# Kernel tuning notes

Hardware: AMD Instinct MI355X
Metric: run time of the kernel (lower is better)

## Reference

```python
import jax, jax.numpy as jnp
import numpy as np
from jax import lax

B, H, W = 2, 960, 1280
K = 1024            # max_keypoints
P = 256             # num_pairs (BAD descriptor dim)
NUM_SCALES = 3
DIFF_ITERS = 3
KAPPA = 0.05
TAU = 0.2           # explicit FED step size (stable < 0.25)
DET_THRESHOLD = 0.001
AKAZE_NMS = 5       # detector-internal NMS window
NMS_WIN = 2 * 3 + 1 # pipeline NMS window (nms_radius=3)
ORI_PATCH = 15
ORI_SIGMA = 2.5
SINK_ITERS = 20
EPSILON = 1.0
UNUSED_SCORE = 1.0
MAX_RADIUS = 5

def _conv(x, k):
    return lax.conv_general_dilated(x, k, (1, 1), 'SAME', dimension_numbers=('NCHW', 'OIHW', 'NCHW'))

_sob = np.array([[-1., 0., 1.], [-2., 0., 2.], [-1., 0., 1.]], np.float32) / 8.0
KX = jnp.asarray(_sob)[None, None]
KY = jnp.asarray(_sob.T)[None, None]
_d2 = np.array([[0., 0., 0.], [1., -2., 1.], [0., 0., 0.]], np.float32)
KXX = jnp.asarray(_d2)[None, None]
KYY = jnp.asarray(_d2.T)[None, None]

# Gaussian weighting kernel for orientation estimation
_c = np.arange(ORI_PATCH, dtype=np.float32) - (ORI_PATCH - 1) / 2.0
_gy, _gx = np.meshgrid(_c, _c, indexing='ij')
_g = np.exp(-(_gx ** 2 + _gy ** 2) / (2.0 * ORI_SIGMA ** 2))
GK = jnp.asarray((_g / _g.sum()).astype(np.float32))[None, None]

# Box-average kernel bank: one normalized box filter per radius 0..MAX_RADIUS
_bc = np.arange(-MAX_RADIUS, MAX_RADIUS + 1, dtype=np.float32)
_by, _bx = np.meshgrid(_bc, _bc, indexing='ij')
_rv = np.arange(MAX_RADIUS + 1, dtype=np.float32)[:, None, None]
_bm = ((np.abs(_by) <= _rv) & (np.abs(_bx) <= _rv)).astype(np.float32)
BOX_BANK = jnp.asarray((_bm / (2.0 * _rv + 1.0) ** 2)[:, None])  # [R+1,1,11,11]

def _shifts(a):
    p = jnp.pad(a, ((0, 0), (0, 0), (1, 1), (1, 1)), mode='edge')
    return p[:, :, :-2, 1:-1], p[:, :, 2:, 1:-1], p[:, :, 1:-1, :-2], p[:, :, 1:-1, 2:]

def _fed_step(L):
    # One explicit Perona-Malik (FED) nonlinear diffusion step
    Lx = _conv(L, KX); Ly = _conv(L, KY)
    g = 1.0 / (1.0 + (Lx * Lx + Ly * Ly) / (KAPPA * KAPPA))
    Ln, Ls, Lw, Le = _shifts(L)
    gn, gs, gw, ge = _shifts(g)
    flux = 0.5 * ((g + gn) * (Ln - L) + (g + gs) * (Ls - L) + (g + gw) * (Lw - L) + (g + ge) * (Le - L))
    return L + TAU * flux

def _maxpool(s, win):
    return lax.reduce_window(s, -jnp.inf, lax.max, (1, win, win), (1, 1, 1), 'SAME')

def _akaze(img):
    # Multi-scale FED diffusion -> Hessian determinant response + orientation map
    L = img
    resp = jnp.zeros((B, H, W), img.dtype)
    for _s in range(NUM_SCALES):
        for _i in range(DIFF_ITERS):
            L = _fed_step(L)
        Lxx = _conv(L, KXX); Lyy = _conv(L, KYY); Lxy = _conv(_conv(L, KX), KY)
        resp = jnp.maximum(resp, (Lxx * Lyy - Lxy * Lxy)[:, 0])
    resp = jnp.where(resp > DET_THRESHOLD, resp, 0.0)
    resp = resp * (resp >= _maxpool(resp, AKAZE_NMS) - 1e-7).astype(resp.dtype)
    gxs = _conv(_conv(img, KX), GK)[:, 0]
    gys = _conv(_conv(img, KY), GK)[:, 0]
    theta = jnp.arctan2(gys, gxs)  # [B,H,W]
    return resp, theta

def _select(resp):
    # Pipeline-level maxpool NMS + top-K selection, pad invalid with (-1,-1)
    mask = (resp >= _maxpool(resp, NMS_WIN) - 1e-7).astype(resp.dtype)
    s = resp * mask
    s = jnp.where(s > 0.0, s, 0.0)
    tk, idx = lax.top_k(s.reshape(B, -1), K)
    y = (idx // W).astype(jnp.float32)
    x = (idx % W).astype(jnp.float32)
    valid = (tk > 0.0).astype(jnp.float32)
    kpts = jnp.where(valid[..., None] > 0.5, jnp.stack([y, x], -1), -1.0)
    return kpts, tk * valid, valid

def _bad(img, kpts, theta, valid, offsets, radii, thresholds):
    # Orientation-aware BAD: box-averaged intensity differences at rotated pair offsets
    bank = _conv(img, BOX_BANK)  # [B,R+1,H,W]
    yc = jnp.clip(kpts[..., 0], 0.0, H - 1.0)
    xc = jnp.clip(kpts[..., 1], 0.0, W - 1.0)
    yi = jnp.round(yc).astype(jnp.int32); xi = jnp.round(xc).astype(jnp.int32)
    th = jax.vmap(lambda m, a, b: m[a, b])(theta, yi, xi)  # [B,K] nearest-sampled orientation
    c = jnp.cos(th)[..., None]; s = jnp.sin(th)[..., None]
    ox1, oy1, ox2, oy2 = offsets[:, 0], offsets[:, 1], offsets[:, 2], offsets[:, 3]
    px1 = xc[..., None] + c * ox1 - s * oy1
    py1 = yc[..., None] + s * ox1 + c * oy1
    px2 = xc[..., None] + c * ox2 - s * oy2
    py2 = yc[..., None] + s * ox2 + c * oy2
    rb = jnp.broadcast_to(radii[None, :], (K, P))
    def samp(px, py):
        xi_ = jnp.clip(jnp.round(px), 0, W - 1).astype(jnp.int32)
        yi_ = jnp.clip(jnp.round(py), 0, H - 1).astype(jnp.int32)
        return jax.vmap(lambda bk, a, b: bk[rb, a, b])(bank, yi_, xi_)  # [B,K,P]
    v = (samp(px1, py1) - samp(px2, py2)) - thresholds[None, None, :]
    v = v * valid[..., None]
    n = jnp.linalg.norm(v, axis=-1, keepdims=True)
    return v / (n + 1e-8)

def _sinkhorn(d1, d2):
    sq1 = jnp.sum(d1 * d1, -1); sq2 = jnp.sum(d2 * d2, -1)
    dist2 = sq1[:, :, None] + sq2[:, None, :] - 2.0 * jnp.einsum('bip,bjp->bij', d1, d2)
    dist = jnp.sqrt(jnp.maximum(dist2, 0.0) + 1e-12)
    Z = jnp.full((B, K + 1, K + 1), UNUSED_SCORE, d1.dtype)
    Z = Z.at[:, :K, :K].set(-dist) / EPSILON
    norm = -jnp.log(2.0 * K)
    log_mu = jnp.concatenate([jnp.zeros(K, Z.dtype), jnp.log(float(K)) * jnp.ones(1, Z.dtype)]) + norm
    log_nu = log_mu
    def body(carry, _):
        u, v = carry
        u = log_mu[None] - jax.nn.logsumexp(Z + v[:, None, :], axis=2)
        v = log_nu[None] - jax.nn.logsumexp(Z + u[:, :, None], axis=1)
        return (u, v), None
    (u, v), _ = lax.scan(body, (jnp.zeros((B, K + 1), Z.dtype), jnp.zeros((B, K + 1), Z.dtype)), None, length=SINK_ITERS)
    return jnp.exp(Z + u[:, :, None] + v[:, None, :] - norm)  # [B,K+1,K+1]

def _forward(img1, img2, offsets, thresholds, radii):
    r1, t1 = _akaze(img1)
    r2, t2 = _akaze(img2)
    k1, s1, v1 = _select(r1)
    k2, s2, v2 = _select(r2)
    d1 = _bad(img1, k1, t1, v1, offsets, radii, thresholds)
    d2 = _bad(img2, k2, t2, v2, offsets, radii, thresholds)
    probs = _sinkhorn(d1, d2)
    return k1, k2, probs

def setup_inputs():
    key = jax.random.key(0)
    k1, k2, k3, k4, k5 = jax.random.split(key, 5)
    img1 = jax.random.uniform(k1, (B, 1, H, W), jnp.float32)
    img2 = jax.random.uniform(k2, (B, 1, H, W), jnp.float32)
    offsets = jax.random.uniform(k3, (P, 4), jnp.float32, -16.0, 16.0)  # box_params - 16
    thresholds = 0.05 * jax.random.normal(k5, (P,), jnp.float32)
    radii = jax.random.randint(k4, (P,), 0, MAX_RADIUS + 1, jnp.int32)
    return {'img1': img1, 'img2': img2, 'offsets': offsets, 'thresholds': thresholds, 'radii': radii}

def reference(img1, img2, offsets, thresholds, radii):
    return _forward(img1, img2, offsets, thresholds, radii)
```

## Files before the change

kernel.cpp:

```cpp
#include <hip/hip_runtime.h>
#include <hip/hip_fp16.h>
#include <math.h>

typedef unsigned long long u64;
typedef unsigned int u32;

#define Hh 960
#define Ww 1280
#define Bb 2
#define Kk 1024
#define Pp 256
#define KP1 1025
#define NSEG 4
#define LISTCAP 131072
#define PR 28
#define PS 57
#define ZLD 1040
#define CANDCAP 8192
static const size_t ZB = (size_t)KP1*ZLD;

static const size_t HWp = (size_t)Hh * Ww;
static const size_t PLn = HWp * Bb;

#define TAUf 0.2f
#define NMS_EPS 1e-7f
#define DET_T 0.001f
#define NORMV (-7.6246189861593985f)
#define LOGKV (6.9314718055994531f)

__constant__ float WR[6] = {1.0f, 1.0f/9.0f, 1.0f/25.0f, 1.0f/49.0f, 1.0f/81.0f, 1.0f/121.0f};

__device__ __forceinline__ int imin(int a,int b){return a<b?a:b;}
__device__ __forceinline__ int imax(int a,int b){return a>b?a:b;}

__global__ __launch_bounds__(256) void fed_step(const float* __restrict__ src, float* __restrict__ dst){
  __shared__ float Lt[36][37];
  __shared__ float Gt[34][35];
  const int bx = blockIdx.x*32, by = blockIdx.y*32, b = blockIdx.z;
  const float* S = src + (size_t)b*HWp;
  float* D = dst + (size_t)b*HWp;
  const int t = threadIdx.y*32 + threadIdx.x;
  for (int i=t;i<36*36;i+=256){
    int ly=i/36, lx=i-ly*36;
    int gy=by+ly-2, gx=bx+lx-2;
    Lt[ly][lx] = (gy>=0 && gy<Hh && gx>=0 && gx<Ww) ? S[(size_t)gy*Ww+gx] : 0.0f;
  }
  __syncthreads();
  const float k2 = (float)(0.05*0.05);
  for (int i=t;i<34*34;i+=256){
    int ly=i/34, lx=i-ly*34;
    int Ly=ly+1, Lx=lx+1;
    float sx = (-Lt[Ly-1][Lx-1]+Lt[Ly-1][Lx+1]
                -2.0f*Lt[Ly][Lx-1]+2.0f*Lt[Ly][Lx+1]
                -Lt[Ly+1][Lx-1]+Lt[Ly+1][Lx+1])*0.125f;
    float sy = (-Lt[Ly-1][Lx-1]-2.0f*Lt[Ly-1][Lx]-Lt[Ly-1][Lx+1]
                +Lt[Ly+1][Lx-1]+2.0f*Lt[Ly+1][Lx]+Lt[Ly+1][Lx+1])*0.125f;
    Gt[ly][lx] = 1.0f/(1.0f + (sx*sx+sy*sy)/k2);
  }
  __syncthreads();
  for (int r=0;r<4;++r){
    int oy=threadIdx.y + r*8, ox=threadIdx.x;
    int gy=by+oy, gx=bx+ox;
    if (gy>=Hh || gx>=Ww) continue;
    int gyn=imax(gy-1,0), gys=imin(gy+1,Hh-1), gxw=imax(gx-1,0), gxe=imin(gx+1,Ww-1);
    float Lc=Lt[oy+2][ox+2];
    float Ln=Lt[gyn-by+2][ox+2];
    float Ls=Lt[gys-by+2][ox+2];
    float Lw=Lt[oy+2][gxw-bx+2];
    float Le=Lt[oy+2][gxe-bx+2];
    float gc=Gt[oy+1][ox+1];
    float gn=Gt[gyn-by+1][ox+1];
    float gs=Gt[gys-by+1][ox+1];
    float gw=Gt[oy+1][gxw-bx+1];
    float ge=Gt[oy+1][gxe-bx+1];
    float flux = 0.5f*((gc+gn)*(Ln-Lc) + (gc+gs)*(Ls-Lc) + (gc+gw)*(Lw-Lc) + (gc+ge)*(Le-Lc));
    D[(size_t)gy*Ww+gx] = Lc + TAUf*flux;
  }
}

__global__ __launch_bounds__(256) void fed_step_resp(const float* __restrict__ src, float* __restrict__ dstL,
                                                     float* __restrict__ resp, int first){
  __shared__ float Lt[40][41];
  __shared__ float Gt[38][39];
  __shared__ float Lp[36][37];
  const int bx=blockIdx.x*32, by=blockIdx.y*32, b=blockIdx.z;
  const int gx0=bx-4, gy0=by-4;
  const float* S=src+(size_t)b*HWp;
  float* DL=dstL+(size_t)b*HWp;
  float* R=resp+(size_t)b*HWp;
  const int t=threadIdx.y*32+threadIdx.x;
  const float k2=(float)(0.05*0.05);
  for(int i=t;i<40*40;i+=256){
    int ly=i/40, lx=i-(i/40)*40;
    int gy=gy0+ly, gx=gx0+lx;
    Lt[ly][lx]=(gy>=0&&gy<Hh&&gx>=0&&gx<Ww)?S[(size_t)gy*Ww+gx]:0.0f;
  }
  __syncthreads();
  for(int i=t;i<38*38;i+=256){
    int y=i/38+1, x=i-(i/38)*38+1;
    float sx=(-Lt[y-1][x-1]+Lt[y-1][x+1]
              -2.0f*Lt[y][x-1]+2.0f*Lt[y][x+1]
              -Lt[y+1][x-1]+Lt[y+1][x+1])*0.125f;
    float sy=(-Lt[y-1][x-1]-2.0f*Lt[y-1][x]-Lt[y-1][x+1]
              +Lt[y+1][x-1]+2.0f*Lt[y+1][x]+Lt[y+1][x+1])*0.125f;
    Gt[y-1][x-1]=1.0f/(1.0f+(sx*sx+sy*sy)/k2);
  }
  __syncthreads();
  for(int i=t;i<36*36;i+=256){
    int y=i/36+2, x=i-(i/36)*36+2;
    int gy=gy0+y, gx=gx0+x;
    float v=0.0f;
    if(gy>=0&&gy<Hh&&gx>=0&&gx<Ww){
      int yn=imax(gy-1,0)-gy0, ys=imin(gy+1,Hh-1)-gy0;
      int xw=imax(gx-1,0)-gx0, xe=imin(gx+1,Ww-1)-gx0;
      float Lc=Lt[y][x];
      float Ln=Lt[yn][x], Ls=Lt[ys][x], Lw=Lt[y][xw], Le=Lt[y][xe];
      float gc=Gt[y-1][x-1], gn=Gt[yn-1][x-1], gs=Gt[ys-1][x-1], gw=Gt[y-1][xw-1], ge=Gt[y-1][xe-1];
      float flux=0.5f*((gc+gn)*(Ln-Lc)+(gc+gs)*(Ls-Lc)+(gc+gw)*(Lw-Lc)+(gc+ge)*(Le-Lc));
      v=Lc+TAUf*flux;
    }
    Lp[y-2][x-2]=v;
  }
  __syncthreads();
  for(int i=t;i<32*32;i+=256){
    int oy=i>>5, ox=i&31;
    DL[(size_t)(by+oy)*Ww+(bx+ox)]=Lp[oy+2][ox+2];
  }
  for(int i=t;i<34*34;i+=256){
    int y=i/34+1, x=i-(i/34)*34+1;
    int gy=gy0+2+y, gx=gx0+2+x;
    float v=0.0f;
    if(gy>=0&&gy<Hh&&gx>=0&&gx<Ww){
      v=(-Lp[y-1][x-1]+Lp[y-1][x+1]
         -2.0f*Lp[y][x-1]+2.0f*Lp[y][x+1]
         -Lp[y+1][x-1]+Lp[y+1][x+1])*0.125f;
    }
    Gt[y-1][x-1]=v;
  }
  __syncthreads();
  for(int i=t;i<32*32;i+=256){
    int oy=i>>5, ox=i&31;
    int y=oy+2, x=ox+2;
    float Lxx=Lp[y][x-1]-2.0f*Lp[y][x]+Lp[y][x+1];
    float Lyy=Lp[y-1][x]-2.0f*Lp[y][x]+Lp[y+1][x];
    float Lxy=(-Gt[y-2][x-2]-2.0f*Gt[y-2][x-1]-Gt[y-2][x]
               +Gt[y][x-2]+2.0f*Gt[y][x-1]+Gt[y][x])*0.125f;
    float det=Lxx*Lyy-Lxy*Lxy;
    size_t id=(size_t)(by+oy)*Ww+(bx+ox);
    R[id]=first?fmaxf(det,0.0f):fmaxf(R[id],det);
  }
}

__global__ __launch_bounds__(256) void detect_compact(const float* __restrict__ resp,
                                                      u64* __restrict__ lists,
                                                      int* __restrict__ cnt, int segbase){
  const int TS=42;
  __shared__ float Tt[TS][TS+1];
  __shared__ float Ss[38][39];
  __shared__ u64 keys[1024];
  __shared__ int lcnt, gbase;
  const int bx = blockIdx.x*32, by = blockIdx.y*32, b = blockIdx.z;
  const float* S = resp + (size_t)b*HWp;
  const int t = threadIdx.y*32 + threadIdx.x;
  if (t==0) lcnt=0;
  for (int i=t;i<TS*TS;i+=256){
    int ly=i/TS, lx=i-ly*TS;
    int gy=by+ly-5, gx=bx+lx-5;
    float v = (gy>=0 && gy<Hh && gx>=0 && gx<Ww) ? S[(size_t)gy*Ww+gx] : 0.0f;
    Tt[ly][lx] = (v>DET_T) ? v : 0.0f;
  }
  __syncthreads();
  for (int i=t;i<38*38;i+=256){
    int ly=i/38, lx=i-ly*38;
    int ty=ly+2, tx=lx+2;
    float m=0.0f;
    #pragma unroll
    for(int dy=-2;dy<=2;dy++)
      #pragma unroll
      for(int dx=-2;dx<=2;dx++)
        m=fmaxf(m,Tt[ty+dy][tx+dx]);
    float c=Tt[ty][tx];
    Ss[ly][lx]=(c>=m-NMS_EPS)?c:0.0f;
  }
  __syncthreads();
  const int seg=segbase+b;
  for (int r=0;r<4;++r){
    int oy=threadIdx.y + r*8, ox=threadIdx.x;
    int gy=by+oy, gx=bx+ox;
    bool pos=false; u64 key=0;
    if (gy<Hh && gx<Ww){
      float v=Ss[oy+3][ox+3];
      if (v>0.0f){
        float m=0.0f;
        #pragma unroll
        for(int dy=0;dy<7;dy++)
          #pragma unroll
          for(int dx=0;dx<7;dx++)
            m=fmaxf(m,Ss[oy+dy][ox+dx]);
        if (v>=m-NMS_EPS){
          u32 idx=(u32)(gy*Ww+gx);
          key=((u64)__float_as_uint(v)<<32)|(u64)(0xFFFFFFFFu-idx);
          pos=true;
        }
      }
    }
    u64 mask=__ballot(pos);
    if (mask){
      int lane=t&63;
      int leader=__ffsll((long long)mask)-1;
      int base=0;
      if (lane==leader) base=atomicAdd(&lcnt,__popcll(mask));
      base=__shfl(base,leader);
      if (pos){
        int rk=__popcll(mask & ((1ULL<<lane)-1ULL));
        keys[base+rk]=key;
      }
    }
  }
  __syncthreads();
  if (t==0 && lcnt>0) gbase=atomicAdd(&cnt[seg*64], lcnt);
  __syncthreads();
  int n=lcnt;
  for (int i=t;i<n;i+=256){
    int p=gbase+i;
    if (p<LISTCAP) lists[(size_t)seg*LISTCAP+p]=keys[i];
  }
}

__global__ __launch_bounds__(256) void topk_hist16(const u64* __restrict__ lists, const int* __restrict__ cnt,
                                                   u32* __restrict__ h16){
  int seg=blockIdx.y;
  int n=imin(cnt[seg*64],LISTCAP);
  const u64* L=lists+(size_t)seg*LISTCAP;
  u32* H=h16+(size_t)seg*65536;
  for(int i=blockIdx.x*256+threadIdx.x;i<n;i+=gridDim.x*256){
    u32 b=(u32)(L[i]>>48);
    atomicAdd(&H[b],1u);
  }
}

__global__ __launch_bounds__(1024) void topk_decide16(const u32* __restrict__ h16, const int* __restrict__ cnt,
                                                      int* __restrict__ b16o, int* __restrict__ krem16,
                                                      int* __restrict__ takeAll, u64* __restrict__ Tf){
  int seg=blockIdx.x, tid=threadIdx.x;
  __shared__ u32 sc[1024];
  const u32* H=h16+(size_t)seg*65536;
  int n=imin(cnt[seg*64],LISTCAP);
  if(n<=Kk){
    if(tid==0){ takeAll[seg]=1; Tf[seg]=1ULL; b16o[seg]=-1; }
    return;
  }
  u32 csum=0;
  u32 hl[64];
  #pragma unroll 8
  for(int j=0;j<64;j++){ hl[j]=H[tid*64+j]; csum+=hl[j]; }
  sc[tid]=csum;
  __syncthreads();
  for(int off=1;off<1024;off<<=1){
    u32 v=(tid+off<1024)?sc[tid+off]:0u;
    __syncthreads();
    sc[tid]+=v;
    __syncthreads();
  }
  u32 nxt=(tid<1023)?sc[tid+1]:0u;
  if(sc[tid]>=(u32)Kk && nxt<(u32)Kk){
    u32 run=nxt;
    for(int j=63;j>=0;j--){
      u32 c=hl[j];
      run+=c;
      if(run>=(u32)Kk){
        b16o[seg]=tid*64+j;
        krem16[seg]=Kk-(int)(run-c);
        takeAll[seg]=0;
        break;
      }
    }
  }
}

__global__ __launch_bounds__(256) void topk_compact(const u64* __restrict__ lists, const int* __restrict__ cnt,
                                                    const int* __restrict__ b16o, const int* __restrict__ takeAll,
                                                    u64* __restrict__ candbuf, int* __restrict__ candcnt){
  int seg=blockIdx.y;
  if(takeAll[seg]) return;
  int n=imin(cnt[seg*64],LISTCAP);
  const u64* L=lists+(size_t)seg*LISTCAP;
  u32 b16=(u32)b16o[seg];
  for(int i0=blockIdx.x*256;i0<n;i0+=gridDim.x*256){
    int i=i0+threadIdx.x;
    bool sel=false; u64 k=0;
    if(i<n){ k=L[i]; sel=((u32)(k>>48)==b16); }
    u64 mask=__ballot(sel);
    if(mask){
      int lane=threadIdx.x&63;
      int leader=__ffsll((long long)mask)-1;
      int base=0;
      if(lane==leader) base=atomicAdd(&candcnt[seg*64],__popcll(mask));
      base=__shfl(base,leader);
      if(sel){
        int p=base+__popcll(mask & ((1ULL<<lane)-1ULL));
        if(p<CANDCAP) candbuf[(size_t)seg*CANDCAP+p]=k;
      }
    }
  }
}

__global__ __launch_bounds__(1024) void topk_finish(const u64* __restrict__ lists, const int* __restrict__ cnt,
                                                    const u64* __restrict__ candbuf, const int* __restrict__ candcnt,
                                                    const int* __restrict__ b16o, const int* __restrict__ krem16,
                                                    const int* __restrict__ takeAll, u64* __restrict__ Tf){
  int seg=blockIdx.x, tid=threadIdx.x;
  if(takeAll[seg]) return;
  __shared__ u64 cands[CANDCAP];
  __shared__ u32 h[256], scan[256];
  __shared__ int bsel;
  int cc=candcnt[seg*64];
  u64 pfx=((u64)(u32)b16o[seg])<<48;
  int kr=krem16[seg];
  if(cc<=CANDCAP){
    for(int i=tid;i<cc;i+=1024) cands[i]=candbuf[(size_t)seg*CANDCAP+i];
    __syncthreads();
    for(int rd=0;rd<6;rd++){
      int shift=40-8*rd;
      u64 maskHi=~0ULL<<(shift+8);
      if(tid<256) h[tid]=0;
      __syncthreads();
      for(int i=tid;i<cc;i+=1024){
        u64 k=cands[i];
        if((k&maskHi)==pfx) atomicAdd(&h[(int)((k>>shift)&255ULL)],1u);
      }
      __syncthreads();
      if(tid<256) scan[tid]=h[tid];
      __syncthreads();
      for(int off=1;off<256;off<<=1){
        u32 v=0;
        if(tid<256 && tid+off<256) v=scan[tid+off];
        __syncthreads();
        if(tid<256) scan[tid]+=v;
        __syncthreads();
      }
      if(tid<256){
        bool ge=(scan[tid]>=(u32)kr);
        bool geN=(tid<255)?(scan[tid+1]>=(u32)kr):false;
        if(ge && !geN) bsel=tid;
      }
      __syncthreads();
      int b=bsel;
      int acc=(b<255)?(int)scan[b+1]:0;
      pfx |= ((u64)(u32)b)<<shift;
      kr -= acc;
      __syncthreads();
    }
  } else {
    int n=imin(cnt[seg*64],LISTCAP);
    const u64* L=lists+(size_t)seg*LISTCAP;
    for(int rd=0;rd<6;rd++){
      int shift=40-8*rd;
      u64 maskHi=~0ULL<<(shift+8);
      if(tid<256) h[tid]=0;
      __syncthreads();
      for(int i=tid;i<n;i+=1024){
        u64 k=L[i];
        if((k&maskHi)==pfx) atomicAdd(&h[(int)((k>>shift)&255ULL)],1u);
      }
      __syncthreads();
      if(tid<256) scan[tid]=h[tid];
      __syncthreads();
      for(int off=1;off<256;off<<=1){
        u32 v=0;
        if(tid<256 && tid+off<256) v=scan[tid+off];
        __syncthreads();
        if(tid<256) scan[tid]+=v;
        __syncthreads();
      }
      if(tid<256){
        bool ge=(scan[tid]>=(u32)kr);
        bool geN=(tid<255)?(scan[tid+1]>=(u32)kr):false;
        if(ge && !geN) bsel=tid;
      }
      __syncthreads();
      int b=bsel;
      int acc=(b<255)?(int)scan[b+1]:0;
      pfx |= ((u64)(u32)b)<<shift;
      kr -= acc;
      __syncthreads();
    }
  }
  if(tid==0) Tf[seg]=pfx;
}

__global__ __launch_bounds__(256) void topk_gather(const u64* __restrict__ lists, const int* __restrict__ cnt,
                                                   const u64* __restrict__ Tf, u64* __restrict__ selbuf,
                                                   int* __restrict__ selcnt){
  int seg=blockIdx.y;
  int n=imin(cnt[seg*64],LISTCAP);
  u64 T=Tf[seg];
  const u64* L=lists+(size_t)seg*LISTCAP;
  for(int i0=blockIdx.x*256;i0<n;i0+=gridDim.x*256){
    int i=i0+threadIdx.x;
    bool sel=false; u64 k=0;
    if(i<n){ k=L[i]; sel=(k>=T); }
    u64 mask=__ballot(sel);
    if(mask){
      int lane=threadIdx.x&63;
      int leader=__ffsll((long long)mask)-1;
      int base=0;
      if(lane==leader) base=atomicAdd(&selcnt[seg*64],__popcll(mask));
      base=__shfl(base,leader);
      if(sel){
        int p=base+__popcll(mask & ((1ULL<<lane)-1ULL));
        if(p<Kk) selbuf[(size_t)seg*Kk+p]=k;
      }
    }
  }
}

__global__ __launch_bounds__(1024) void finalize_kernel(const u64* __restrict__ selbuf, const int* __restrict__ selcnt,
                                int* __restrict__ kyi, int* __restrict__ kxi, float* __restrict__ kval,
                                float* __restrict__ outp){
  int seg=blockIdx.x, tid=threadIdx.x;
  __shared__ u64 a[1024];
  int n=selcnt[seg*64]; if(n>Kk)n=Kk;
  a[tid]=(tid<n)?selbuf[(size_t)seg*Kk+tid]:0ULL;
  __syncthreads();
  for(int k=2;k<=1024;k<<=1){
    for(int j=k>>1;j>0;j>>=1){
      int ixj=tid^j;
      if(ixj>tid){
        u64 x=a[tid], y=a[ixj];
        bool desc=((tid&k)==0);
        if(desc ? (x<y) : (x>y)){ a[tid]=y; a[ixj]=x; }
      }
      __syncthreads();
    }
  }
  u64 key=a[tid];
  bool val=(key!=0ULL);
  u32 idx=0xFFFFFFFFu-(u32)(key&0xFFFFFFFFULL);
  int y= val ? (int)(idx/Ww) : 0;
  int x= val ? (int)(idx%Ww) : 0;
  int mi=seg*Kk+tid;
  kyi[mi]=y; kxi[mi]=x; kval[mi]= val?1.0f:0.0f;
  int imi=seg>>1, bb=seg&1;
  float* ko=outp + (size_t)imi*(Bb*Kk*2) + ((size_t)bb*Kk+tid)*2;
  ko[0]= val ? (float)y : -1.0f;
  ko[1]= val ? (float)x : -1.0f;
}

__global__ void init_weights(float* wn){
  if(threadIdx.x==0 && blockIdx.x==0){
    double w[15]; double S=0.0;
    for(int i=0;i<15;i++){ double c=(double)i-7.0; w[i]=exp(-(c*c)/(2.0*2.5*2.5)); S+=w[i]; }
    for(int i=0;i<15;i++) wn[i]=(float)(w[i]/S);
  }
}

__global__ __launch_bounds__(256) void bad_kernel(const float* __restrict__ img1, const float* __restrict__ img2,
                           const float* __restrict__ offs, const float* __restrict__ thrv,
                           const int* __restrict__ rad, const float* __restrict__ wn,
                           const int* __restrict__ kyi, const int* __restrict__ kxi,
                           const float* __restrict__ kval,
                           float* __restrict__ d1, float* __restrict__ d2,
                           float* __restrict__ sq1, float* __restrict__ sq2){
  __shared__ float sat[PS+1][PS+2];
  __shared__ float sm[4], smx[4], smy[4];
  __shared__ float w15s[15];
  __shared__ float nsh, thsh;
  int seg=blockIdx.y, ki=blockIdx.x, p=threadIdx.x;
  const float* img=(seg<2?img1:img2)+(size_t)(seg&1)*HWp;
  int mi=seg*Kk+ki;
  int yci=kyi[mi], xci=kxi[mi];
  if(p<15) w15s[p]=wn[p];
  for (int i=p;i<PS+1;i+=256){ sat[0][i]=0.0f; sat[i][0]=0.0f; }
  if (p==0) sat[0][PS]=0.0f;
  for (int i=p;i<PS*PS;i+=256){
    int ly=i/PS, lx=i-ly*PS;
    int gy=yci-PR+ly, gx=xci-PR+lx;
    sat[ly+1][lx+1]=(gy>=0&&gy<Hh&&gx>=0&&gx<Ww)?img[(size_t)gy*Ww+gx]:0.0f;
  }
  __syncthreads();
  {
    float ax=0.0f, ay=0.0f;
    if(p<225){
      int du=p/15-7, dv=p-(p/15)*15-7;
      int yy=yci+du, xx=xci+dv;
      if(yy>=0&&yy<Hh&&xx>=0&&xx<Ww){
        int ly=du+PR+1, lx=dv+PR+1;
        float p00=sat[ly-1][lx-1], p01=sat[ly-1][lx], p02=sat[ly-1][lx+1];
        float p10=sat[ly][lx-1],                       p12=sat[ly][lx+1];
        float p20=sat[ly+1][lx-1], p21=sat[ly+1][lx], p22=sat[ly+1][lx+1];
        float sx=(-p00+p02-2.0f*p10+2.0f*p12-p20+p22)*0.125f;
        float sy=(-p00-2.0f*p01-p02+p20+2.0f*p21+p22)*0.125f;
        float wgt=w15s[du+7]*w15s[dv+7];
        ax=wgt*sx; ay=wgt*sy;
      }
    }
    for(int o=32;o;o>>=1){ ax+=__shfl_down(ax,o); ay+=__shfl_down(ay,o); }
    if((p&63)==0){ smx[p>>6]=ax; smy[p>>6]=ay; }
    __syncthreads();
    if(p==0) thsh=atan2f(smy[0]+smy[1]+smy[2]+smy[3], smx[0]+smx[1]+smx[2]+smx[3]);
  }
  __syncthreads();
  if (p<PS){
    float run=0.0f;
    for(int x=1;x<=PS;x++){ run+=sat[p+1][x]; sat[p+1][x]=run; }
  }
  __syncthreads();
  if (p<PS){
    float run=0.0f;
    for(int y=1;y<=PS;y++){ run+=sat[y][p+1]; sat[y][p+1]=run; }
  }
  __syncthreads();
  float yc=(float)yci, xc=(float)xci;
  float th=thsh;
  float c=cosf(th), s=sinf(th);
  float ox1=offs[p*4+0], oy1=offs[p*4+1], ox2=offs[p*4+2], oy2=offs[p*4+3];
  int r=rad[p];
  float w=WR[r];
  float px1=xc+c*ox1-s*oy1, py1=yc+s*ox1+c*oy1;
  float px2=xc+c*ox2-s*oy2, py2=yc+s*ox2+c*oy2;
  auto boxl=[&](float px,float py,int r_)->float{
    float rx=rintf(px), ry=rintf(py);
    int xi=(int)fminf(fmaxf(rx,0.0f),(float)(Ww-1));
    int yi=(int)fminf(fmaxf(ry,0.0f),(float)(Hh-1));
    int lx=xi-(xci-PR), ly=yi-(yci-PR);
    int y2=ly+r_+1, y1=ly-r_, x2=lx+r_+1, x1=lx-r_;
    return sat[y2][x2]-sat[y1][x2]-sat[y2][x1]+sat[y1][x1];
  };
  float s1=boxl(px1,py1,r)*w;
  float s2=boxl(px2,py2,r)*w;
  float v=(s1-s2-thrv[p])*kval[mi];
  float t=v*v;
  for(int o=32;o;o>>=1) t+=__shfl_down(t,o);
  if((p&63)==0) sm[p>>6]=t;
  __syncthreads();
  if(p==0) nsh=sqrtf(sm[0]+sm[1]+sm[2]+sm[3]);
  __syncthreads();
  float dv=v/(nsh+1e-8f);
  float* dd=(seg<2?d1:d2);
  dd[((size_t)(seg&1)*Kk+ki)*Pp+p]=dv;
  float t2=dv*dv;
  for(int o=32;o;o>>=1) t2+=__shfl_down(t2,o);
  __syncthreads();
  if((p&63)==0) sm[p>>6]=t2;
  __syncthreads();
  if(p==0){ float* sq=(seg<2?sq1:sq2); sq[(size_t)(seg&1)*Kk+ki]=sm[0]+sm[1]+sm[2]+sm[3]; }
}

__global__ __launch_bounds__(256) void dist_kernel(const float* __restrict__ d1, const float* __restrict__ d2,
                            const float* __restrict__ sq1, const float* __restrict__ sq2,
                            float* __restrict__ Zm, float* __restrict__ Zt){
  int b=blockIdx.z;
  int i0=blockIdx.y*64, j0=blockIdx.x*64;
  int tid=threadIdx.x;
  int tx=tid&15, ty=tid>>4;
  __shared__ float Ast[64][68], Bst[64][68];
  const float* D1=d1+(size_t)b*Kk*Pp;
  const float* D2=d2+(size_t)b*Kk*Pp;
  float acc[4][4]={};
  for(int p0=0;p0<Pp;p0+=64){
    for(int i=tid;i<64*16;i+=256){
      int row=i>>4, c4=(i&15)<<2;
      float4 va=*reinterpret_cast<const float4*>(&D1[(size_t)(i0+row)*Pp+p0+c4]);
      float4 vb=*reinterpret_cast<const float4*>(&D2[(size_t)(j0+row)*Pp+p0+c4]);
      Ast[c4+0][row]=va.x; Ast[c4+1][row]=va.y; Ast[c4+2][row]=va.z; Ast[c4+3][row]=va.w;
      Bst[c4+0][row]=vb.x; Bst[c4+1][row]=vb.y; Bst[c4+2][row]=vb.z; Bst[c4+3][row]=vb.w;
    }
    __syncthreads();
    #pragma unroll 8
    for(int kk=0;kk<64;++kk){
      float4 av=*reinterpret_cast<const float4*>(&Ast[kk][ty*4]);
      float4 bv=*reinterpret_cast<const float4*>(&Bst[kk][tx*4]);
      acc[0][0]=fmaf(av.x,bv.x,acc[0][0]); acc[0][1]=fmaf(av.x,bv.y,acc[0][1]);
      acc[0][2]=fmaf(av.x,bv.z,acc[0][2]); acc[0][3]=fmaf(av.x,bv.w,acc[0][3]);
      acc[1][0]=fmaf(av.y,bv.x,acc[1][0]); acc[1][1]=fmaf(av.y,bv.y,acc[1][1]);
      acc[1][2]=fmaf(av.y,bv.z,acc[1][2]); acc[1][3]=fmaf(av.y,bv.w,acc[1][3]);
      acc[2][0]=fmaf(av.z,bv.x,acc[2][0]); acc[2][1]=fmaf(av.z,bv.y,acc[2][1]);
      acc[2][2]=fmaf(av.z,bv.z,acc[2][2]); acc[2][3]=fmaf(av.z,bv.w,acc[2][3]);
      acc[3][0]=fmaf(av.w,bv.x,acc[3][0]); acc[3][1]=fmaf(av.w,bv.y,acc[3][1]);
      acc[3][2]=fmaf(av.w,bv.z,acc[3][2]); acc[3][3]=fmaf(av.w,bv.w,acc[3][3]);
    }
    __syncthreads();
  }
  int gi=i0+ty*4, gj=j0+tx*4;
  float si[4], sj[4];
  #pragma unroll
  for(int i=0;i<4;i++){ si[i]=sq1[b*Kk+gi+i]; sj[i]=sq2[b*Kk+gj+i]; }
  #pragma unroll
  for(int i=0;i<4;i++){
    #pragma unroll
    for(int j=0;j<4;j++){
      float dd=si[i]+sj[j]-2.0f*acc[i][j];
      float dist=sqrtf(fmaxf(dd,0.0f)+1e-12f);
      Zm[(size_t)b*ZB+(size_t)(gi+i)*ZLD+(gj+j)]=-dist;
      Zt[(size_t)b*ZB+(size_t)(gj+j)*ZLD+(gi+i)]=-dist;
    }
  }
}

__global__ void zborder_kernel(float* __restrict__ Zm, float* __restrict__ Zt){
  int i=blockIdx.x*256+threadIdx.x;
  if(i>=Bb*KP1) return;
  int b=i/KP1, j=i-(i/KP1)*KP1;
  size_t base=(size_t)b*ZB;
  Zm[base+(size_t)j*ZLD+Kk]=1.0f;
  Zm[base+(size_t)Kk*ZLD+j]=1.0f;
  Zt[base+(size_t)j*ZLD+Kk]=1.0f;
  Zt[base+(size_t)Kk*ZLD+j]=1.0f;
  for(int c=KP1;c<ZLD;c++){
    Zm[base+(size_t)j*ZLD+c]=-1.0e30f;
    Zt[base+(size_t)j*ZLD+c]=-1.0e30f;
  }
}

__global__ void expz_kernel(const float* __restrict__ Zm, const float* __restrict__ Zt,
                            __half* __restrict__ Em, __half* __restrict__ Et){
  size_t q=(size_t)blockIdx.x*256+threadIdx.x;
  const size_t tot4=(size_t)Bb*ZB/4;
  if(q>=2*tot4) return;
  const float* src=(q<tot4)?Zm:Zt;
  __half* dst=(q<tot4)?Em:Et;
  size_t j=(q<tot4)?q:q-tot4;
  float4 z=reinterpret_cast<const float4*>(src)[j];
  __half2 a=__floats2half2_rn(expf(z.x),expf(z.y));
  __half2 b=__floats2half2_rn(expf(z.z),expf(z.w));
  reinterpret_cast<__half2*>(dst)[2*j]=a;
  reinterpret_cast<__half2*>(dst)[2*j+1]=b;
}

__global__ void init_euv(float* __restrict__ euv, float* __restrict__ evv){
  int i=blockIdx.x*256+threadIdx.x;
  if(i>=Bb*ZLD) return;
  int j=i-(i/ZLD)*ZLD;
  evv[i]=(j<KP1)?1.0f:0.0f;
  euv[i]=0.0f;
}

struct H4{ __half2 a, b; };
__global__ __launch_bounds__(256) void sink_gemv(const __half* __restrict__ E,
        const float* __restrict__ evin, float* __restrict__ euout, float* __restrict__ uout){
  int row=blockIdx.x*4+(threadIdx.x>>6);
  if(row>=Bb*KP1) return;
  int b=row/KP1, i=row-b*KP1;
  int lane=threadIdx.x&63;
  const H4* e4=reinterpret_cast<const H4*>(E+((size_t)b*KP1+i)*ZLD);
  const float4* v4=reinterpret_cast<const float4*>(evin+(size_t)b*ZLD);
  float s=0.0f;
  for(int j=lane;j<ZLD/4;j+=64){
    H4 e=e4[j]; float4 v=v4[j];
    float2 ea=__half22float2(e.a), eb=__half22float2(e.b);
    s=fmaf(ea.x,v.x,s); s=fmaf(ea.y,v.y,s);
    s=fmaf(eb.x,v.z,s); s=fmaf(eb.y,v.w,s);
  }
  for(int o=32;o;o>>=1) s+=__shfl_down(s,o);
  if(lane==0){
    float lm,elm;
    if(i<Kk){ lm=NORMV; elm=4.8828125e-4f; }
    else    { lm=LOGKV+NORMV; elm=0.5f; }
    euout[(size_t)b*ZLD+i]=elm/s;
    uout [(size_t)b*ZLD+i]=lm-logf(s);
  }
}

__global__ void probs_kernel(const float* __restrict__ Zm, const float* __restrict__ uu,
                             const float* __restrict__ vv, float* __restrict__ outp){
  size_t i=(size_t)blockIdx.x*256+threadIdx.x;
  const size_t tot=(size_t)Bb*KP1*KP1;
  if(i>=tot) return;
  size_t b=i/((size_t)KP1*KP1);
  size_t rem=i-b*(size_t)KP1*KP1;
  int rr=(int)(rem/KP1), cc=(int)(rem-(size_t)(rem/KP1)*KP1);
  outp[i]=expf(Zm[b*ZB+(size_t)rr*ZLD+cc]+uu[b*ZLD+rr]+vv[b*ZLD+cc]-NORMV);
}

extern "C" void kernel_launch(void* const* d_in, const int* in_sizes, int n_in,
                              void* d_out, int out_size, void* d_ws, size_t ws_size,
                              hipStream_t stream) {
  (void)in_sizes; (void)n_in; (void)out_size;
  const float* img1=(const float*)d_in[0];
  const float* img2=(const float*)d_in[1];
  const float* offs=(const float*)d_in[2];
  const float* thrv=(const float*)d_in[3];
  const int*   rad =(const int*)d_in[4];
  float* out=(float*)d_out;

  const bool batched = ws_size >= ((size_t)80<<20);
  const int NP = batched ? 4 : 2;
  const size_t PB = HWp*(size_t)NP*4;

  char* wp=(char*)d_ws;
  auto carve=[&](size_t bytes)->char*{ char* p=wp; wp += (bytes+255)&~(size_t)255; return p; };
  float* r0  =(float*)carve(PB);
  float* r1  =(float*)carve(PB);
  float* resp=(float*)carve(PB);
  u64*  lists=(u64*)carve((size_t)NSEG*LISTCAP*8);
  char* stateblk = carve(8192);
  int* cnt     =(int*)(stateblk);
  int* selcnt  =(int*)(stateblk+1024);
  int* b16o    =(int*)(stateblk+2048);
  int* krem16  =(int*)(stateblk+2112);
  int* takeAll =(int*)(stateblk+2176);
  u64* Tf      =(u64*)(stateblk+2240);
  int* candcnt =(int*)(stateblk+4096);
  u32* h16     =(u32*)carve((size_t)NSEG*65536*4);
  u64* candbuf =(u64*)carve((size_t)NSEG*CANDCAP*8);
  u64* selbuf  =(u64*)carve((size_t)NSEG*Kk*8);
  int* kyi     =(int*)carve((size_t)NSEG*Kk*4);
  int* kxi     =(int*)carve((size_t)NSEG*Kk*4);
  float* kval  =(float*)carve((size_t)NSEG*Kk*4);
  float* d1    =(float*)carve((size_t)Bb*Kk*Pp*4);
  float* d2    =(float*)carve((size_t)Bb*Kk*Pp*4);
  float* sq1   =(float*)carve((size_t)Bb*Kk*4);
  float* sq2   =(float*)carve((size_t)Bb*Kk*4);
  float* uvec  =(float*)carve((size_t)Bb*ZLD*4);
  float* vvec  =(float*)carve((size_t)Bb*ZLD*4);
  float* euvec =(float*)carve((size_t)Bb*ZLD*4);
  float* evvec =(float*)carve((size_t)Bb*ZLD*4);
  float* wn    =(float*)carve(64);

  const size_t EBYTES = ((size_t)Bb*ZB*2 + 255)&~(size_t)255;
  __half* Em=(__half*)resp;
  __half* Et=(__half*)((char*)resp + EBYTES);

  hipMemsetAsync(stateblk, 0, 8192, stream);
  hipMemsetAsync(h16, 0, (size_t)NSEG*65536*4, stream);
  init_weights<<<1,32,0,stream>>>(wn);

  dim3 TB(32,8);
  if (batched){
    dim3 TG(Ww/32, Hh/32, 4);
    hipMemcpyAsync(r0,       img1, PLn*4, hipMemcpyDeviceToDevice, stream);
    hipMemcpyAsync(r0+2*HWp, img2, PLn*4, hipMemcpyDeviceToDevice, stream);
    float* cur=r0; float* oth=r1;
    for(int st=1; st<=9; ++st){
      if(st%3==0) fed_step_resp<<<TG,TB,0,stream>>>(cur, oth, resp, st==3);
      else        fed_step<<<TG,TB,0,stream>>>(cur, oth);
      float* tp=cur; cur=oth; oth=tp;
    }
    detect_compact<<<TG,TB,0,stream>>>(resp, lists, cnt, 0);
  } else {
    dim3 TG(Ww/32, Hh/32, Bb);
    for(int im=0; im<2; ++im){
      const float* srcimg = (im==0)? img1 : img2;
      hipMemcpyAsync(r0, srcimg, PLn*4, hipMemcpyDeviceToDevice, stream);
      float* cur=r0; float* oth=r1;
      for(int st=1; st<=9; ++st){
        if(st%3==0) fed_step_resp<<<TG,TB,0,stream>>>(cur, oth, resp, st==3);
        else        fed_step<<<TG,TB,0,stream>>>(cur, oth);
        float* tp=cur; cur=oth; oth=tp;
      }
      detect_compact<<<TG,TB,0,stream>>>(resp, lists, cnt, im*2);
    }
  }

  topk_hist16 <<<dim3(32,NSEG),dim3(256),0,stream>>>(lists, cnt, h16);
  topk_decide16<<<dim3(NSEG),dim3(1024),0,stream>>>(h16, cnt, b16o, krem16, takeAll, Tf);
  topk_compact<<<dim3(32,NSEG),dim3(256),0,stream>>>(lists, cnt, b16o, takeAll, candbuf, candcnt);
  topk_finish <<<dim3(NSEG),dim3(1024),0,stream>>>(lists, cnt, candbuf, candcnt, b16o, krem16, takeAll, Tf);
  topk_gather <<<dim3(32,NSEG),dim3(256),0,stream>>>(lists, cnt, Tf, selbuf, selcnt);
  finalize_kernel<<<NSEG,1024,0,stream>>>(selbuf, selcnt, kyi, kxi, kval, out);
  bad_kernel<<<dim3(Kk,NSEG),dim3(256),0,stream>>>(img1, img2, offs, thrv, rad, wn,
                                                   kyi, kxi, kval, d1, d2, sq1, sq2);

  float* Zm=r0; float* Zt=r1;
  dist_kernel<<<dim3(16,16,Bb),dim3(256),0,stream>>>(d1,d2,sq1,sq2,Zm,Zt);
  zborder_kernel<<<dim3((Bb*KP1+255)/256),dim3(256),0,stream>>>(Zm,Zt);
  {
    size_t tot4=(size_t)Bb*ZB/4;
    expz_kernel<<<dim3((u32)((2*tot4+255)/256)),dim3(256),0,stream>>>(Zm,Zt,Em,Et);
  }
  init_euv<<<dim3((Bb*ZLD+255)/256),dim3(256),0,stream>>>(euvec,evvec);
  for(int it=0; it<20; ++it){
    sink_gemv<<<dim3((Bb*KP1+3)/4),dim3(256),0,stream>>>(Em, evvec, euvec, uvec);
    sink_gemv<<<dim3((Bb*KP1+3)/4),dim3(256),0,stream>>>(Et, euvec, evvec, vvec);
  }
  size_t tot=(size_t)Bb*KP1*KP1;
  probs_kernel<<<dim3((u32)((tot+255)/256)),dim3(256),0,stream>>>(Zm, uvec, vvec, out + (size_t)2*Bb*Kk*2);
}
```

Baseline: 596.1 us.

## Fuse paired FED steps, bitmask NMS, and fold border/weight kernels

Fuses two consecutive FED diffusion steps into one kernel with a wider halo, and reads the input images directly instead of copying them first in batched mode. This removes a global-memory round trip and a launch per fused pair. Detection NMS now keeps a per-row ballot bitmask and only visits surviving candidates, and the per-tile key buffer shrinks to a capped size. The Gaussian weight init and Z border kernels are folded into bad_kernel and expz_kernel to drop launches. The trade-offs are redundant halo computation, possible dropped keypoints if a tile has more candidates than the cap, and every bad_kernel block recomputing the weights in double precision.

Measured after the change: 567.2 us. 1.05x faster.

```diff
diff --git a/kernel.cpp b/kernel.cpp
--- a/kernel.cpp
+++ b/kernel.cpp
@@ -17,6 +17,7 @@
 #define PS 57
 #define ZLD 1040
 #define CANDCAP 8192
+#define KEYCAP 256
 static const size_t ZB = (size_t)KP1*ZLD;
 
 static const size_t HWp = (size_t)Hh * Ww;
@@ -33,48 +34,64 @@
 __device__ __forceinline__ int imin(int a,int b){return a<b?a:b;}
 __device__ __forceinline__ int imax(int a,int b){return a>b?a:b;}
 
-__global__ __launch_bounds__(256) void fed_step(const float* __restrict__ src, float* __restrict__ dst){
-  __shared__ float Lt[36][37];
-  __shared__ float Gt[34][35];
-  const int bx = blockIdx.x*32, by = blockIdx.y*32, b = blockIdx.z;
-  const float* S = src + (size_t)b*HWp;
-  float* D = dst + (size_t)b*HWp;
-  const int t = threadIdx.y*32 + threadIdx.x;
-  for (int i=t;i<36*36;i+=256){
-    int ly=i/36, lx=i-ly*36;
-    int gy=by+ly-2, gx=bx+lx-2;
-    Lt[ly][lx] = (gy>=0 && gy<Hh && gx>=0 && gx<Ww) ? S[(size_t)gy*Ww+gx] : 0.0f;
-  }
-  __syncthreads();
-  const float k2 = (float)(0.05*0.05);
-  for (int i=t;i<34*34;i+=256){
-    int ly=i/34, lx=i-ly*34;
-    int Ly=ly+1, Lx=lx+1;
-    float sx = (-Lt[Ly-1][Lx-1]+Lt[Ly-1][Lx+1]
-                -2.0f*Lt[Ly][Lx-1]+2.0f*Lt[Ly][Lx+1]
-                -Lt[Ly+1][Lx-1]+Lt[Ly+1][Lx+1])*0.125f;
-    float sy = (-Lt[Ly-1][Lx-1]-2.0f*Lt[Ly-1][Lx]-Lt[Ly-1][Lx+1]
-                +Lt[Ly+1][Lx-1]+2.0f*Lt[Ly+1][Lx]+Lt[Ly+1][Lx+1])*0.125f;
-    Gt[ly][lx] = 1.0f/(1.0f + (sx*sx+sy*sy)/k2);
-  }
-  __syncthreads();
-  for (int r=0;r<4;++r){
-    int oy=threadIdx.y + r*8, ox=threadIdx.x;
+__global__ __launch_bounds__(256) void fed2_step(const float* __restrict__ src, float* __restrict__ dst,
+                const float* __restrict__ img1, const float* __restrict__ img2, int fromImgs){
+  __shared__ float Lt[40][41];
+  __shared__ float Gt[38][39];
+  __shared__ float Lp[36][37];
+  const int bx=blockIdx.x*32, by=blockIdx.y*32, b=blockIdx.z;
+  const int gx0=bx-4, gy0=by-4;
+  const float* S = fromImgs ? ((b<2?img1:img2)+(size_t)(b&1)*HWp) : (src+(size_t)b*HWp);
+  float* D=dst+(size_t)b*HWp;
+  const int t=threadIdx.y*32+threadIdx.x;
+  const float k2=(float)(0.05*0.05);
+  for(int i=t;i<40*40;i+=256){
+    int ly=i/40, lx=i-(i/40)*40;
+    int gy=gy0+ly, gx=gx0+lx;
+    Lt[ly][lx]=(gy>=0&&gy<Hh&&gx>=0&&gx<Ww)?S[(size_t)gy*Ww+gx]:0.0f;
+  }
+  __syncthreads();
+  for(int i=t;i<38*38;i+=256){
+    int y=i/38+1, x=i-(i/38)*38+1;
+    float sx=(-Lt[y-1][x-1]+Lt[y-1][x+1]-2.0f*Lt[y][x-1]+2.0f*Lt[y][x+1]-Lt[y+1][x-1]+Lt[y+1][x+1])*0.125f;
+    float sy=(-Lt[y-1][x-1]-2.0f*Lt[y-1][x]-Lt[y-1][x+1]+Lt[y+1][x-1]+2.0f*Lt[y+1][x]+Lt[y+1][x+1])*0.125f;
+    Gt[y-1][x-1]=1.0f/(1.0f+(sx*sx+sy*sy)/k2);
+  }
+  __syncthreads();
+  for(int i=t;i<36*36;i+=256){
+    int y=i/36+2, x=i-(i/36)*36+2;
+    int gy=gy0+y, gx=gx0+x;
+    float v=0.0f;
+    if(gy>=0&&gy<Hh&&gx>=0&&gx<Ww){
+      int yn=imax(gy-1,0)-gy0, ys=imin(gy+1,Hh-1)-gy0;
+      int xw=imax(gx-1,0)-gx0, xe=imin(gx+1,Ww-1)-gx0;
+      float Lc=Lt[y][x];
+      float Ln=Lt[yn][x], Ls=Lt[ys][x], Lw=Lt[y][xw], Le=Lt[y][xe];
+      float gc=Gt[y-1][x-1], gn=Gt[yn-1][x-1], gs=Gt[ys-1][x-1], gw=Gt[y-1][xw-1], ge=Gt[y-1][xe-1];
+      float flux=0.5f*((gc+gn)*(Ln-Lc)+(gc+gs)*(Ls-Lc)+(gc+gw)*(Lw-Lc)+(gc+ge)*(Le-Lc));
+      v=Lc+TAUf*flux;
+    }
+    Lp[y-2][x-2]=v;
+  }
+  __syncthreads();
+  for(int i=t;i<34*34;i+=256){
+    int y=i/34+1, x=i-(i/34)*34+1;
+    float sx=(-Lp[y-1][x-1]+Lp[y-1][x+1]-2.0f*Lp[y][x-1]+2.0f*Lp[y][x+1]-Lp[y+1][x-1]+Lp[y+1][x+1])*0.125f;
+    float sy=(-Lp[y-1][x-1]-2.0f*Lp[y-1][x]-Lp[y-1][x+1]+Lp[y+1][x-1]+2.0f*Lp[y+1][x]+Lp[y+1][x+1])*0.125f;
+    Gt[y-1][x-1]=1.0f/(1.0f+(sx*sx+sy*sy)/k2);
+  }
+  __syncthreads();
+  for(int i=t;i<32*32;i+=256){
+    int oy=i>>5, ox=i&31;
+    int y=oy+2, x=ox+2;
     int gy=by+oy, gx=bx+ox;
-    if (gy>=Hh || gx>=Ww) continue;
-    int gyn=imax(gy-1,0), gys=imin(gy+1,Hh-1), gxw=imax(gx-1,0), gxe=imin(gx+1,Ww-1);
-    float Lc=Lt[oy+2][ox+2];
-    float Ln=Lt[gyn-by+2][ox+2];
-    float Ls=Lt[gys-by+2][ox+2];
-    float Lw=Lt[oy+2][gxw-bx+2];
-    float Le=Lt[oy+2][gxe-bx+2];
-    float gc=Gt[oy+1][ox+1];
-    float gn=Gt[gyn-by+1][ox+1];
-    float gs=Gt[gys-by+1][ox+1];
-    float gw=Gt[oy+1][gxw-bx+1];
-    float ge=Gt[oy+1][gxe-bx+1];
-    float flux = 0.5f*((gc+gn)*(Ln-Lc) + (gc+gs)*(Ls-Lc) + (gc+gw)*(Lw-Lc) + (gc+ge)*(Le-Lc));
-    D[(size_t)gy*Ww+gx] = Lc + TAUf*flux;
+    int yn=imax(gy-1,0)-(gy0+2), ys=imin(gy+1,Hh-1)-(gy0+2);
+    int xw=imax(gx-1,0)-(gx0+2), xe=imin(gx+1,Ww-1)-(gx0+2);
+    float Lc=Lp[y][x];
+    float Ln=Lp[yn][x], Ls=Lp[ys][x], Lw=Lp[y][xw], Le=Lp[y][xe];
+    float gc=Gt[y-1][x-1], gn=Gt[yn-1][x-1], gs=Gt[ys-1][x-1], gw=Gt[y-1][xw-1], ge=Gt[y-1][xe-1];
+    float flux=0.5f*((gc+gn)*(Ln-Lc)+(gc+gs)*(Ls-Lc)+(gc+gw)*(Lw-Lc)+(gc+ge)*(Le-Lc));
+    D[(size_t)gy*Ww+gx]=Lc+TAUf*flux;
   }
 }
 
@@ -156,8 +173,8 @@
                                                       int* __restrict__ cnt, int segbase){
   const int TS=42;
   __shared__ float Tt[TS][TS+1];
-  __shared__ float Ss[38][39];
-  __shared__ u64 keys[1024];
+  __shared__ u64 bm[38];
+  __shared__ u64 keys[KEYCAP];
   __shared__ int lcnt, gbase;
   const int bx = blockIdx.x*32, by = blockIdx.y*32, b = blockIdx.z;
   const float* S = resp + (size_t)b*HWp;
@@ -170,38 +187,45 @@
     Tt[ly][lx] = (v>DET_T) ? v : 0.0f;
   }
   __syncthreads();
-  for (int i=t;i<38*38;i+=256){
-    int ly=i/38, lx=i-ly*38;
-    int ty=ly+2, tx=lx+2;
-    float m=0.0f;
-    #pragma unroll
-    for(int dy=-2;dy<=2;dy++)
-      #pragma unroll
-      for(int dx=-2;dx<=2;dx++)
-        m=fmaxf(m,Tt[ty+dy][tx+dx]);
-    float c=Tt[ty][tx];
-    Ss[ly][lx]=(c>=m-NMS_EPS)?c:0.0f;
+  {
+    int wave=t>>6, lane=t&63;
+    for(int y=wave; y<38; y+=4){
+      bool pred=false;
+      if(lane<38){
+        float m=0.0f;
+        #pragma unroll
+        for(int dy=0;dy<5;dy++)
+          #pragma unroll
+          for(int dx=0;dx<5;dx++)
+            m=fmaxf(m,Tt[y+dy][lane+dx]);
+        float c=Tt[y+2][lane+2];
+        pred=(c>0.0f)&&(c>=m-NMS_EPS);
+      }
+      u64 mask=__ballot(pred);
+      if(lane==0) bm[y]=mask;
+    }
   }
   __syncthreads();
   const int seg=segbase+b;
   for (int r=0;r<4;++r){
     int oy=threadIdx.y + r*8, ox=threadIdx.x;
-    int gy=by+oy, gx=bx+ox;
     bool pos=false; u64 key=0;
-    if (gy<Hh && gx<Ww){
-      float v=Ss[oy+3][ox+3];
-      if (v>0.0f){
-        float m=0.0f;
-        #pragma unroll
-        for(int dy=0;dy<7;dy++)
-          #pragma unroll
-          for(int dx=0;dx<7;dx++)
-            m=fmaxf(m,Ss[oy+dy][ox+dx]);
-        if (v>=m-NMS_EPS){
-          u32 idx=(u32)(gy*Ww+gx);
-          key=((u64)__float_as_uint(v)<<32)|(u64)(0xFFFFFFFFu-idx);
-          pos=true;
+    if((bm[oy+3]>>(ox+3))&1ULL){
+      float v=Tt[oy+5][ox+5];
+      float m=0.0f;
+      #pragma unroll
+      for(int dy=0;dy<7;dy++){
+        u32 chunk=(u32)((bm[oy+dy]>>ox)&0x7FULL);
+        while(chunk){
+          int j=__ffs(chunk)-1;
+          m=fmaxf(m,Tt[oy+dy+2][ox+j+2]);
+          chunk&=chunk-1;
         }
+      }
+      if(v>=m-NMS_EPS){
+        u32 idx=(u32)((by+oy)*Ww+(bx+ox));
+        key=((u64)__float_as_uint(v)<<32)|(u64)(0xFFFFFFFFu-idx);
+        pos=true;
       }
     }
     u64 mask=__ballot(pos);
@@ -213,14 +237,14 @@
       base=__shfl(base,leader);
       if (pos){
         int rk=__popcll(mask & ((1ULL<<lane)-1ULL));
-        keys[base+rk]=key;
-      }
-    }
-  }
-  __syncthreads();
-  if (t==0 && lcnt>0) gbase=atomicAdd(&cnt[seg*64], lcnt);
-  __syncthreads();
-  int n=lcnt;
+        if(base+rk<KEYCAP) keys[base+rk]=key;
+      }
+    }
+  }
+  __syncthreads();
+  int n=imin(lcnt,KEYCAP);
+  if (t==0 && n>0) gbase=atomicAdd(&cnt[seg*64], n);
+  __syncthreads();
   for (int i=t;i<n;i+=256){
     int p=gbase+i;
     if (p<LISTCAP) lists[(size_t)seg*LISTCAP+p]=keys[i];
@@ -447,17 +471,9 @@
   ko[1]= val ? (float)x : -1.0f;
 }
 
-__global__ void init_weights(float* wn){
-  if(threadIdx.x==0 && blockIdx.x==0){
-    double w[15]; double S=0.0;
-    for(int i=0;i<15;i++){ double c=(double)i-7.0; w[i]=exp(-(c*c)/(2.0*2.5*2.5)); S+=w[i]; }
-    for(int i=0;i<15;i++) wn[i]=(float)(w[i]/S);
-  }
-}
-
 __global__ __launch_bounds__(256) void bad_kernel(const float* __restrict__ img1, const float* __restrict__ img2,
                            const float* __restrict__ offs, const float* __restrict__ thrv,
-                           const int* __restrict__ rad, const float* __restrict__ wn,
+                           const int* __restrict__ rad,
                            const int* __restrict__ kyi, const int* __restrict__ kxi,
                            const float* __restrict__ kval,
                            float* __restrict__ d1, float* __restrict__ d2,
@@ -470,7 +486,11 @@
   const float* img=(seg<2?img1:img2)+(size_t)(seg&1)*HWp;
   int mi=seg*Kk+ki;
   int yci=kyi[mi], xci=kxi[mi];
-  if(p<15) w15s[p]=wn[p];
+  if(p==0){
+    double w[15]; double Sw=0.0;
+    for(int i=0;i<15;i++){ double c=(double)i-7.0; w[i]=exp(-(c*c)/(2.0*2.5*2.5)); Sw+=w[i]; }
+    for(int i=0;i<15;i++) w15s[i]=(float)(w[i]/Sw);
+  }
   for (int i=p;i<PS+1;i+=256){ sat[0][i]=0.0f; sat[i][0]=0.0f; }
   if (p==0) sat[0][PS]=0.0f;
   for (int i=p;i<PS*PS;i+=256){
@@ -598,34 +618,36 @@
   }
 }
 
-__global__ void zborder_kernel(float* __restrict__ Zm, float* __restrict__ Zt){
-  int i=blockIdx.x*256+threadIdx.x;
-  if(i>=Bb*KP1) return;
-  int b=i/KP1, j=i-(i/KP1)*KP1;
-  size_t base=(size_t)b*ZB;
-  Zm[base+(size_t)j*ZLD+Kk]=1.0f;
-  Zm[base+(size_t)Kk*ZLD+j]=1.0f;
-  Zt[base+(size_t)j*ZLD+Kk]=1.0f;
-  Zt[base+(size_t)Kk*ZLD+j]=1.0f;
-  for(int c=KP1;c<ZLD;c++){
-    Zm[base+(size_t)j*ZLD+c]=-1.0e30f;
-    Zt[base+(size_t)j*ZLD+c]=-1.0e30f;
-  }
-}
-
-__global__ void expz_kernel(const float* __restrict__ Zm, const float* __restrict__ Zt,
+__global__ void expz_kernel(float* __restrict__ Zm, float* __restrict__ Zt,
                             __half* __restrict__ Em, __half* __restrict__ Et){
   size_t q=(size_t)blockIdx.x*256+threadIdx.x;
   const size_t tot4=(size_t)Bb*ZB/4;
   if(q>=2*tot4) return;
-  const float* src=(q<tot4)?Zm:Zt;
+  float* src=(q<tot4)?Zm:Zt;
   __half* dst=(q<tot4)?Em:Et;
   size_t j=(q<tot4)?q:q-tot4;
+  size_t jb=j%(ZB/4);
+  int r=(int)(jb/(ZLD/4));
+  int c0=(int)(jb%(ZLD/4))*4;
   float4 z=reinterpret_cast<const float4*>(src)[j];
-  __half2 a=__floats2half2_rn(expf(z.x),expf(z.y));
-  __half2 b=__floats2half2_rn(expf(z.z),expf(z.w));
+  float zz[4]={z.x,z.y,z.z,z.w};
+  float e[4];
+  bool wb=false;
+  #pragma unroll
+  for(int k=0;k<4;k++){
+    int c=c0+k;
+    if(c>=KP1) e[k]=0.0f;
+    else if(r==Kk||c==Kk){ zz[k]=1.0f; e[k]=expf(1.0f); wb=true; }
+    else e[k]=expf(zz[k]);
+  }
+  if(wb){
+    float4 zo; zo.x=zz[0]; zo.y=zz[1]; zo.z=zz[2]; zo.w=zz[3];
+    reinterpret_cast<float4*>(src)[j]=zo;
+  }
+  __half2 a=__floats2half2_rn(e[0],e[1]);
+  __half2 b2=__floats2half2_rn(e[2],e[3]);
   reinterpret_cast<__half2*>(dst)[2*j]=a;
-  reinterpret_cast<__half2*>(dst)[2*j+1]=b;
+  reinterpret_cast<__half2*>(dst)[2*j+1]=b2;
 }
 
 __global__ void init_euv(float* __restrict__ euv, float* __restrict__ evv){
@@ -716,7 +738,6 @@
   float* vvec  =(float*)carve((size_t)Bb*ZLD*4);
   float* euvec =(float*)carve((size_t)Bb*ZLD*4);
   float* evvec =(float*)carve((size_t)Bb*ZLD*4);
-  float* wn    =(float*)carve(64);
 
   const size_t EBYTES = ((size_t)Bb*ZB*2 + 255)&~(size_t)255;
   __half* Em=(__half*)resp;
@@ -724,31 +745,28 @@
 
   hipMemsetAsync(stateblk, 0, 8192, stream);
   hipMemsetAsync(h16, 0, (size_t)NSEG*65536*4, stream);
-  init_weights<<<1,32,0,stream>>>(wn);
 
   dim3 TB(32,8);
   if (batched){
     dim3 TG(Ww/32, Hh/32, 4);
-    hipMemcpyAsync(r0,       img1, PLn*4, hipMemcpyDeviceToDevice, stream);
-    hipMemcpyAsync(r0+2*HWp, img2, PLn*4, hipMemcpyDeviceToDevice, stream);
-    float* cur=r0; float* oth=r1;
-    for(int st=1; st<=9; ++st){
-      if(st%3==0) fed_step_resp<<<TG,TB,0,stream>>>(cur, oth, resp, st==3);
-      else        fed_step<<<TG,TB,0,stream>>>(cur, oth);
-      float* tp=cur; cur=oth; oth=tp;
-    }
+    fed2_step   <<<TG,TB,0,stream>>>(r0, r1, img1, img2, 1);
+    fed_step_resp<<<TG,TB,0,stream>>>(r1, r0, resp, 1);
+    fed2_step   <<<TG,TB,0,stream>>>(r0, r1, img1, img2, 0);
+    fed_step_resp<<<TG,TB,0,stream>>>(r1, r0, resp, 0);
+    fed2_step   <<<TG,TB,0,stream>>>(r0, r1, img1, img2, 0);
+    fed_step_resp<<<TG,TB,0,stream>>>(r1, r0, resp, 0);
     detect_compact<<<TG,TB,0,stream>>>(resp, lists, cnt, 0);
   } else {
     dim3 TG(Ww/32, Hh/32, Bb);
     for(int im=0; im<2; ++im){
       const float* srcimg = (im==0)? img1 : img2;
       hipMemcpyAsync(r0, srcimg, PLn*4, hipMemcpyDeviceToDevice, stream);
-      float* cur=r0; float* oth=r1;
-      for(int st=1; st<=9; ++st){
-        if(st%3==0) fed_step_resp<<<TG,TB,0,stream>>>(cur, oth, resp, st==3);
-        else        fed_step<<<TG,TB,0,stream>>>(cur, oth);
-        float* tp=cur; cur=oth; oth=tp;
-      }
+      fed2_step   <<<TG,TB,0,stream>>>(r0, r1, img1, img2, 0);
+      fed_step_resp<<<TG,TB,0,stream>>>(r1, r0, resp, 1);
+      fed2_step   <<<TG,TB,0,stream>>>(r0, r1, img1, img2, 0);
+      fed_step_resp<<<TG,TB,0,stream>>>(r1, r0, resp, 0);
+      fed2_step   <<<TG,TB,0,stream>>>(r0, r1, img1, img2, 0);
+      fed_step_resp<<<TG,TB,0,stream>>>(r1, r0, resp, 0);
       detect_compact<<<TG,TB,0,stream>>>(resp, lists, cnt, im*2);
     }
   }
@@ -759,12 +777,11 @@
   topk_finish <<<dim3(NSEG),dim3(1024),0,stream>>>(lists, cnt, candbuf, candcnt, b16o, krem16, takeAll, Tf);
   topk_gather <<<dim3(32,NSEG),dim3(256),0,stream>>>(lists, cnt, Tf, selbuf, selcnt);
   finalize_kernel<<<NSEG,1024,0,stream>>>(selbuf, selcnt, kyi, kxi, kval, out);
-  bad_kernel<<<dim3(Kk,NSEG),dim3(256),0,stream>>>(img1, img2, offs, thrv, rad, wn,
+  bad_kernel<<<dim3(Kk,NSEG),dim3(256),0,stream>>>(img1, img2, offs, thrv, rad,
                                                    kyi, kxi, kval, d1, d2, sq1, sq2);
 
   float* Zm=r0; float* Zt=r1;
   dist_kernel<<<dim3(16,16,Bb),dim3(256),0,stream>>>(d1,d2,sq1,sq2,Zm,Zt);
-  zborder_kernel<<<dim3((Bb*KP1+255)/256),dim3(256),0,stream>>>(Zm,Zt);
   {
     size_t tot4=(size_t)Bb*ZB/4;
     expz_kernel<<<dim3((u32)((2*tot4+255)/256)),dim3(256),0,stream>>>(Zm,Zt,Em,Et);
```
